# Kernel tuning notes

Measured on AMD Instinct MI355X. Metric: run time of the kernel, lower is better.

The kernel has to match this reference:

```python
import jax, jax.numpy as jnp
import numpy as np

NUM_HEADS = 8
EPS = 1e-9


def setup_inputs() -> dict:
    key = jax.random.key(0)
    ks = jax.random.split(key, 5)
    B, S, D = 2, 2048, 512
    x = jax.random.normal(ks[0], (B, S, D), dtype=jnp.float32)
    Wq = jax.random.normal(ks[1], (D, D), dtype=jnp.float32) * (1.0 / np.sqrt(D))
    Wk = jax.random.normal(ks[2], (D, D), dtype=jnp.float32) * (1.0 / np.sqrt(D))
    Wv = jax.random.normal(ks[3], (D, D), dtype=jnp.float32) * (1.0 / np.sqrt(D))
    Wo = jax.random.normal(ks[4], (D, D), dtype=jnp.float32) * (1.0 / np.sqrt(D))
    gamma = jnp.ones((D,), dtype=jnp.float32)
    beta = jnp.zeros((D,), dtype=jnp.float32)
    return {"x": x, "Wq": Wq, "Wk": Wk, "Wv": Wv, "Wo": Wo, "gamma": gamma, "beta": beta}


def _layernorm(x, gamma, beta):
    mean = jnp.mean(x, axis=-1, keepdims=True)
    var = jnp.mean(jnp.square(x - mean), axis=-1, keepdims=True)
    return gamma * ((x - mean) * jax.lax.rsqrt(var + EPS)) + beta


def reference(x, Wq, Wk, Wv, Wo, gamma, beta):
    B, S, D = x.shape
    H = NUM_HEADS
    dh = D // H
    # Note: in the original, K_V=(inputs, inputs) is captured BEFORE LayerNorm,
    # so only Q is layer-normalized; K and V use the raw inputs.
    q_in = _layernorm(x, gamma, beta)
    Q = jnp.einsum('bsd,de->bse', q_in, Wq).reshape(B, S, H, dh)
    K = jnp.einsum('bsd,de->bse', x, Wk).reshape(B, S, H, dh)
    V = jnp.einsum('bsd,de->bse', x, Wv).reshape(B, S, H, dh)
    # scaled dot-product attention (bias = 0, dropout disabled since dropout=1)
    scores = jnp.einsum('bqhd,bkhd->bhqk', Q, K) / jnp.sqrt(jnp.float32(dh))
    attn = jax.nn.softmax(scores, axis=-1)
    ctx = jnp.einsum('bhqk,bkhd->bqhd', attn, V).reshape(B, S, D)
    out = jnp.einsum('bsd,de->bse', ctx, Wo) + x  # output proj + residual
    return out
```

## Files before the change

kernel.cpp:

```cpp
#include <hip/hip_runtime.h>

typedef __bf16 bf16x8 __attribute__((ext_vector_type(8)));
typedef float f32x4 __attribute__((ext_vector_type(4)));

#define SCALE_LOG2E 0.18033688011112042f

__device__ __forceinline__ float bf2f(unsigned int u) { return __uint_as_float(u << 16); }
__device__ __forceinline__ unsigned short f2bfu(float f) {
    union { __bf16 h; unsigned short u; } v;
    v.h = (__bf16)f;
    return v.u;
}
__device__ __forceinline__ unsigned int pk2bf(float a, float b) {
    union { __bf16 h[2]; unsigned int u; } v;
    v.h[0] = (__bf16)a; v.h[1] = (__bf16)b;
    return v.u;
}

__device__ int probe_bf16(const void* xp) {
    const unsigned short* u = (const unsigned short*)xp;
    int cnt = 0;
    for (int i = 0; i < 128; i++) {
        unsigned e = (u[i] >> 7) & 0xFFu;
        cnt += (e == 0u || (e >= 0x6Cu && e <= 0x8Au)) ? 1 : 0;
    }
    return cnt >= 120;
}

__global__ __launch_bounds__(64)
void probe_k(const void* __restrict__ x, const void* __restrict__ Wq, int* __restrict__ flags) {
    if (threadIdx.x == 0) {
        flags[0] = probe_bf16(x);
        flags[1] = probe_bf16(Wq);
    }
}

__device__ __forceinline__ void load8f(const void* p, int isb, size_t idx, float* o) {
    if (isb) {
        uint4 v = *(const uint4*)((const unsigned short*)p + idx);
        o[0] = bf2f(v.x & 0xffffu); o[1] = bf2f(v.x >> 16);
        o[2] = bf2f(v.y & 0xffffu); o[3] = bf2f(v.y >> 16);
        o[4] = bf2f(v.z & 0xffffu); o[5] = bf2f(v.z >> 16);
        o[6] = bf2f(v.w & 0xffffu); o[7] = bf2f(v.w >> 16);
    } else {
        const float* f = (const float*)p + idx;
        float4 a = *(const float4*)f;
        float4 b = *(const float4*)(f + 4);
        o[0] = a.x; o[1] = a.y; o[2] = a.z; o[3] = a.w;
        o[4] = b.x; o[5] = b.y; o[6] = b.z; o[7] = b.w;
    }
}
__device__ __forceinline__ void load2f(const void* p, int isb, size_t idx, float& a, float& b) {
    if (isb) {
        unsigned int v = *(const unsigned int*)((const unsigned short*)p + idx);
        a = bf2f(v & 0xffffu); b = bf2f(v >> 16);
    } else {
        float2 f = *(const float2*)((const float*)p + idx);
        a = f.x; b = f.y;
    }
}
__device__ __forceinline__ float load1f(const void* p, int isb, size_t idx) {
    return isb ? bf2f((unsigned int)((const unsigned short*)p)[idx]) : ((const float*)p)[idx];
}

__global__ __launch_bounds__(256)
void setup_k(const void* __restrict__ x, const void* __restrict__ Wq, const void* __restrict__ Wk,
             const void* __restrict__ Wv, const void* __restrict__ Wo,
             const void* __restrict__ gamma, const void* __restrict__ beta,
             float* __restrict__ rowstats, float* __restrict__ gf, float* __restrict__ bfv,
             unsigned short* __restrict__ WT, const int* __restrict__ flags) {
    const int t = threadIdx.x;
    const int bid = blockIdx.x;
    if (bid < 1024) {
        const int isb = flags[1];
        __shared__ float tile[32][33];
        const int which = bid >> 8, tl = bid & 255;
        const int bx = (tl & 15) * 32, by = (tl >> 4) * 32;
        const void* W = (which == 0) ? Wq : (which == 1) ? Wk : (which == 2) ? Wv : Wo;
        unsigned short* dst = WT + (size_t)which * 512 * 512;
        const int xx = t & 31, y0 = t >> 5;
#pragma unroll
        for (int i = 0; i < 4; i++) {
            int y = y0 + i * 8;
            tile[y][xx] = load1f(W, isb, (size_t)(by + y) * 512 + bx + xx);
        }
        __syncthreads();
#pragma unroll
        for (int i = 0; i < 4; i++) {
            int y = y0 + i * 8;
            dst[(size_t)(bx + y) * 512 + by + xx] = f2bfu(tile[xx][y]);
        }
        return;
    }
    const int isb = flags[0];
    if (bid >= 5120) {
        const void* src = (bid == 5120) ? gamma : beta;
        float* dst = (bid == 5120) ? gf : bfv;
        float a, b;
        load2f(src, isb, (size_t)t * 2, a, b);
        dst[t * 2] = a; dst[t * 2 + 1] = b;
        return;
    }
    const int row = bid - 1024;
    float a, b;
    load2f(x, isb, (size_t)row * 512 + t * 2, a, b);
    float s = a + b, sq = a * a + b * b;
#pragma unroll
    for (int msk = 1; msk < 64; msk <<= 1) {
        s += __shfl_xor(s, msk);
        sq += __shfl_xor(sq, msk);
    }
    __shared__ float red[8];
    if ((t & 63) == 0) { red[t >> 6] = s; red[4 + (t >> 6)] = sq; }
    __syncthreads();
    if (t == 0) {
        float S = red[0] + red[1] + red[2] + red[3];
        float SQ = red[4] + red[5] + red[6] + red[7];
        float mean = S * (1.0f / 512.0f);
        float var = SQ * (1.0f / 512.0f) - mean * mean;
        rowstats[2 * row] = mean;
        rowstats[2 * row + 1] = rsqrtf(fmaxf(var, 0.0f) + 1e-9f);
    }
}

__global__ __launch_bounds__(256)
void proj_all_k(const void* __restrict__ x, const unsigned short* __restrict__ WT,
                const float* __restrict__ rowstats, const float* __restrict__ gf,
                const float* __restrict__ bfv, unsigned short* __restrict__ Qb,
                unsigned short* __restrict__ Kb, unsigned short* __restrict__ VtF,
                const int* __restrict__ flags) {
    __shared__ unsigned short As[128 * 40];
    __shared__ unsigned short Bs[128 * 40];
    __shared__ float Gs[512], Bts[512];
    const int t = threadIdx.x;
    const int isb = flags[0];
    const int w = t >> 6, lane = t & 63;
    const int quad = lane >> 4, ln = lane & 15;

    if (blockIdx.z == 0) {
        const int role = blockIdx.x & 1;
        const int n0 = (blockIdx.x >> 1) * 128;
        const int m0 = blockIdx.y * 128;
        const unsigned short* BT = WT + (size_t)role * 512 * 512;
        unsigned short* out = role ? Kb : Qb;
        const int wm = w & 1, wn = w >> 1;
        Gs[t] = gf[t]; Gs[t + 256] = gf[t + 256];
        Bts[t] = bfv[t]; Bts[t + 256] = bfv[t + 256];

        f32x4 acc[4][4];
        const f32x4 zero = {0.f, 0.f, 0.f, 0.f};
#pragma unroll
        for (int i = 0; i < 4; i++)
#pragma unroll
            for (int j = 0; j < 4; j++) acc[i][j] = zero;

        for (int kt = 0; kt < 512; kt += 32) {
            __syncthreads();
#pragma unroll
            for (int i = 0; i < 2; i++) {
                int o = t + i * 256;
                int r = o >> 2, c8 = o & 3;
                size_t gidx = (size_t)(m0 + r) * 512 + kt + c8 * 8;
                if (isb && role == 1) {
                    *(uint4*)(&As[r * 40 + c8 * 8]) = *(const uint4*)((const unsigned short*)x + gidx);
                } else {
                    float f[8];
                    load8f(x, isb, gidx, f);
                    if (role == 0) {
                        float mean = rowstats[2 * (m0 + r)];
                        float inv = rowstats[2 * (m0 + r) + 1];
#pragma unroll
                        for (int j = 0; j < 8; j++) {
                            int k = kt + c8 * 8 + j;
                            f[j] = (f[j] - mean) * inv * Gs[k] + Bts[k];
                        }
                    }
                    unsigned int pk[4];
#pragma unroll
                    for (int j = 0; j < 4; j++) pk[j] = pk2bf(f[2 * j], f[2 * j + 1]);
                    *(uint4*)(&As[r * 40 + c8 * 8]) = make_uint4(pk[0], pk[1], pk[2], pk[3]);
                }
                *(uint4*)(&Bs[r * 40 + c8 * 8]) = *(const uint4*)(BT + (size_t)(n0 + r) * 512 + kt + c8 * 8);
            }
            __syncthreads();
            bf16x8 af[4], bfr[4];
#pragma unroll
            for (int i = 0; i < 4; i++) {
                af[i] = *(const bf16x8*)(&As[(wm * 64 + i * 16 + ln) * 40 + quad * 8]);
                bfr[i] = *(const bf16x8*)(&Bs[(wn * 64 + i * 16 + ln) * 40 + quad * 8]);
            }
#pragma unroll
            for (int i = 0; i < 4; i++)
#pragma unroll
                for (int j = 0; j < 4; j++)
                    acc[i][j] = __builtin_amdgcn_mfma_f32_16x16x32_bf16(af[i], bfr[j], acc[i][j], 0, 0, 0);
        }
#pragma unroll
        for (int i = 0; i < 4; i++)
#pragma unroll
            for (int j = 0; j < 4; j++)
#pragma unroll
                for (int r = 0; r < 4; r++) {
                    int grow = m0 + wm * 64 + i * 16 + quad * 4 + r;
                    int gcol = n0 + wn * 64 + j * 16 + ln;
                    float v = acc[i][j][r];
                    if (role == 0) v *= SCALE_LOG2E;
                    out[(size_t)grow * 512 + gcol] = f2bfu(v);
                }
    } else {
        const int m0 = blockIdx.x * 64;
        const int n0 = blockIdx.y * 128;
        const unsigned short* AW = WT + (size_t)2 * 512 * 512;

        f32x4 acc[8];
        const f32x4 zero = {0.f, 0.f, 0.f, 0.f};
#pragma unroll
        for (int j = 0; j < 8; j++) acc[j] = zero;

        for (int kt = 0; kt < 512; kt += 32) {
            __syncthreads();
            {
                int r = t >> 2, c8 = t & 3;
                *(uint4*)(&As[r * 40 + c8 * 8]) = *(const uint4*)(AW + (size_t)(m0 + r) * 512 + kt + c8 * 8);
            }
#pragma unroll
            for (int i = 0; i < 2; i++) {
                int o = t + i * 256;
                int r = o >> 2, c8 = o & 3;
                size_t gidx = (size_t)(n0 + r) * 512 + kt + c8 * 8;
                if (isb) {
                    *(uint4*)(&Bs[r * 40 + c8 * 8]) = *(const uint4*)((const unsigned short*)x + gidx);
                } else {
                    float f[8];
                    load8f(x, isb, gidx, f);
                    unsigned int pk[4];
#pragma unroll
                    for (int j = 0; j < 4; j++) pk[j] = pk2bf(f[2 * j], f[2 * j + 1]);
                    *(uint4*)(&Bs[r * 40 + c8 * 8]) = make_uint4(pk[0], pk[1], pk[2], pk[3]);
                }
            }
            __syncthreads();
            bf16x8 af = *(const bf16x8*)(&As[(w * 16 + ln) * 40 + quad * 8]);
#pragma unroll
            for (int j = 0; j < 8; j++) {
                bf16x8 bfr = *(const bf16x8*)(&Bs[(j * 16 + ln) * 40 + quad * 8]);
                acc[j] = __builtin_amdgcn_mfma_f32_16x16x32_bf16(af, bfr, acc[j], 0, 0, 0);
            }
        }
#pragma unroll
        for (int j = 0; j < 8; j++)
#pragma unroll
            for (int r = 0; r < 4; r++) {
                int grow = m0 + w * 16 + quad * 4 + r;
                int gcol = n0 + j * 16 + ln;
                VtF[(size_t)grow * 4096 + gcol] = f2bfu(acc[j][r]);
            }
    }
}

__global__ __launch_bounds__(1024, 8)
void attn_m_k(const unsigned short* __restrict__ Qb, const unsigned short* __restrict__ Kb,
              const unsigned short* __restrict__ VtF, unsigned short* __restrict__ ctx) {
    const int S = 2048, PT = 72;
    const int t = threadIdx.x;
    const int qb = blockIdx.x, h = blockIdx.y, b = blockIdx.z;
    const int w = t >> 6, lane = t & 63;
    const int quad = lane >> 4, ln = lane & 15;
    const int qs = w & 3, kq = w >> 2;
    const int kh2 = kq & 1, ntp = kq >> 1;

    __shared__ unsigned short sh[384 * 72];
    unsigned short* const Qs  = sh;
    unsigned short* const KsA = sh + 64 * 72;
    unsigned short* const KsB = sh + 128 * 72;
    unsigned short* const VtA = sh + 192 * 72;
    unsigned short* const VtB = sh + 256 * 72;
    unsigned short* const PsA = sh;
    unsigned short* const PsB = sh + 320 * 72;

    const size_t baseQ  = (size_t)(b * S + qb * 64) * 512 + h * 64;
    const size_t baseK  = (size_t)(b * S) * 512 + h * 64;
    const size_t baseVt = (size_t)(h * 64) * 4096 + (size_t)b * S;

    const int r64 = (t & 511) >> 3, c8 = t & 7;

    const int stoff = r64 * PT + c8 * 8;
    const int kfo0  = (kq * 16 + ln) * PT + quad * 8;
    const int pso   = (qs * 16 + ln) * PT + kq * 16 + quad * 4;
    const int apo   = (qs * 16 + ln) * PT + kh2 * 32 + quad * 8;
    const int vbo0  = (ntp * 2 * 16 + ln) * PT + kh2 * 32 + quad * 8;

    const unsigned short* const gK = Kb + baseK + (size_t)r64 * 512 + c8 * 8;
    const unsigned short* const gV = VtF + baseVt + (size_t)r64 * 4096 + c8 * 8;

    if (t < 512)
        *(uint4*)(&Qs[stoff]) = *(const uint4*)(Qb + baseQ + (size_t)r64 * 512 + c8 * 8);
    __syncthreads();
    bf16x8 qf[2];
#pragma unroll
    for (int i = 0; i < 2; i++)
        qf[i] = *(const bf16x8*)(&Qs[(qs * 16 + ln) * PT + quad * 8 + 32 * i]);

    f32x4 acc[2];
    const f32x4 zero = {0.f, 0.f, 0.f, 0.f};
    acc[0] = zero; acc[1] = zero;
    float lsum = 0.f;

    uint4 sreg;
    if (t < 512) sreg = *(const uint4*)(gK);
    else         sreg = *(const uint4*)(gV);

#define ATTN_TILE(KS, VT, PS, ...)                                                      \
    {                                                                                   \
        if (t < 512) *(uint4*)(&KS[stoff]) = sreg;                                      \
        else         *(uint4*)(&VT[stoff]) = sreg;                                      \
        __syncthreads();                                           \
        __VA_ARGS__                                      \
        f32x4 sc = zero;                                                                \
        sc = __builtin_amdgcn_mfma_f32_16x16x32_bf16(                                   \
            *(const bf16x8*)(&KS[kfo0]), qf[0], sc, 0, 0, 0);                           \
        sc = __builtin_amdgcn_mfma_f32_16x16x32_bf16(                                   \
            *(const bf16x8*)(&KS[kfo0 + 32]), qf[1], sc, 0, 0, 0);                      \
        float e0 = __builtin_amdgcn_exp2f(fminf(sc[0], 30.f));                          \
        float e1 = __builtin_amdgcn_exp2f(fminf(sc[1], 30.f));                          \
        float e2 = __builtin_amdgcn_exp2f(fminf(sc[2], 30.f));                          \
        float e3 = __builtin_amdgcn_exp2f(fminf(sc[3], 30.f));                          \
        lsum += (e0 + e1) + (e2 + e3);                                                  \
        *(uint2*)(&PS[pso]) = make_uint2(pk2bf(e0, e1), pk2bf(e2, e3));                 \
        __syncthreads();                 \
        bf16x8 ap = *(const bf16x8*)(&PS[apo]);                                         \
        acc[0] = __builtin_amdgcn_mfma_f32_16x16x32_bf16(                               \
            ap, *(const bf16x8*)(&VT[vbo0]), acc[0], 0, 0, 0);                          \
        acc[1] = __builtin_amdgcn_mfma_f32_16x16x32_bf16(                               \
            ap, *(const bf16x8*)(&VT[vbo0 + 16 * PT]), acc[1], 0, 0, 0);                \
    }

    for (int kc = 0; kc < S; kc += 128) {
        ATTN_TILE(KsA, VtA, PsA, {
            if (t < 512) sreg = *(const uint4*)(gK + (size_t)(kc + 64) * 512);
            else         sreg = *(const uint4*)(gV + kc + 64);
        })
        ATTN_TILE(KsB, VtB, PsB, {
            if (kc + 128 < S) {
                if (t < 512) sreg = *(const uint4*)(gK + (size_t)(kc + 128) * 512);
                else         sreg = *(const uint4*)(gV + kc + 128);
            }
        })
    }
#undef ATTN_TILE

    lsum += __shfl_xor(lsum, 16);
    lsum += __shfl_xor(lsum, 32);

    __syncthreads();
    float* scr  = (float*)sh;
    float* lred = scr + 4096;
    if (quad == 0) lred[kq * 64 + qs * 16 + ln] = lsum;
    if (kh2 == 1) {
#pragma unroll
        for (int ntl = 0; ntl < 2; ntl++)
#pragma unroll
            for (int r = 0; r < 4; r++)
                scr[(qs * 16 + quad * 4 + r) * 64 + (ntp * 2 + ntl) * 16 + ln] = acc[ntl][r];
    }
    __syncthreads();
    if (kh2 == 0) {
        const size_t baseO = (size_t)(b * S + qb * 64 + qs * 16 + quad * 4) * 512 + h * 64 + ln;
#pragma unroll
        for (int r = 0; r < 4; r++) {
            int qrow = qs * 16 + quad * 4 + r;
            float lt = lred[qrow] + lred[64 + qrow] + lred[128 + qrow] + lred[192 + qrow];
            float inv = 1.0f / lt;
#pragma unroll
            for (int ntl = 0; ntl < 2; ntl++) {
                int nt = ntp * 2 + ntl;
                float v = acc[ntl][r] + scr[qrow * 64 + nt * 16 + ln];
                ctx[baseO + (size_t)r * 512 + nt * 16] = f2bfu(v * inv);
            }
        }
    }
}

__global__ __launch_bounds__(256)
void outproj_k(const unsigned short* __restrict__ ctx, const unsigned short* __restrict__ BT,
               const void* __restrict__ x, void* __restrict__ outp, const int* __restrict__ flags) {
    __shared__ unsigned short As[128 * 40];
    __shared__ unsigned short Bs[64 * 40];
    const int t = threadIdx.x;
    const int isb = flags[0];
    const int m0 = blockIdx.y * 128, n0 = blockIdx.x * 64;
    const int w = t >> 6, lane = t & 63;
    const int wm = w & 1, wn = w >> 1;
    const int quad = lane >> 4, ln = lane & 15;

    f32x4 acc[4][2];
    const f32x4 zero = {0.f, 0.f, 0.f, 0.f};
#pragma unroll
    for (int i = 0; i < 4; i++)
#pragma unroll
        for (int j = 0; j < 2; j++) acc[i][j] = zero;

    for (int kt = 0; kt < 512; kt += 32) {
        __syncthreads();
#pragma unroll
        for (int i = 0; i < 2; i++) {
            int o = t + i * 256;
            int r = o >> 2, c8 = o & 3;
            *(uint4*)(&As[r * 40 + c8 * 8]) = *(const uint4*)(ctx + (size_t)(m0 + r) * 512 + kt + c8 * 8);
        }
        {
            int r = t >> 2, c8 = t & 3;
            *(uint4*)(&Bs[r * 40 + c8 * 8]) = *(const uint4*)(BT + (size_t)(n0 + r) * 512 + kt + c8 * 8);
        }
        __syncthreads();
        bf16x8 af[4], bfr[2];
#pragma unroll
        for (int i = 0; i < 4; i++)
            af[i] = *(const bf16x8*)(&As[(wm * 64 + i * 16 + ln) * 40 + quad * 8]);
#pragma unroll
        for (int j = 0; j < 2; j++)
            bfr[j] = *(const bf16x8*)(&Bs[(wn * 32 + j * 16 + ln) * 40 + quad * 8]);
#pragma unroll
        for (int i = 0; i < 4; i++)
#pragma unroll
            for (int j = 0; j < 2; j++)
                acc[i][j] = __builtin_amdgcn_mfma_f32_16x16x32_bf16(af[i], bfr[j], acc[i][j], 0, 0, 0);
    }
#pragma unroll
    for (int i = 0; i < 4; i++)
#pragma unroll
        for (int j = 0; j < 2; j++)
#pragma unroll
            for (int r = 0; r < 4; r++) {
                int grow = m0 + wm * 64 + i * 16 + quad * 4 + r;
                int gcol = n0 + wn * 32 + j * 16 + ln;
                size_t idx = (size_t)grow * 512 + gcol;
                float v = acc[i][j][r] + load1f(x, isb, idx);
                if (isb) ((unsigned short*)outp)[idx] = f2bfu(v);
                else     ((float*)outp)[idx] = v;
            }
}

__global__ __launch_bounds__(256)
void fill_k(unsigned short* out, int n) {
    int i = blockIdx.x * 256 + threadIdx.x;
    if (i < n) out[i] = 0x4442;
}

extern "C" void kernel_launch(void* const* d_in, const int* in_sizes, int n_in,
                              void* d_out, int out_size, void* d_ws, size_t ws_size,
                              hipStream_t stream) {
    const void* x     = d_in[0];
    const void* Wq    = d_in[1];
    const void* Wk    = d_in[2];
    const void* Wv    = d_in[3];
    const void* Wo    = d_in[4];
    const void* gamma = d_in[5];
    const void* beta  = d_in[6];

    const size_t NW = 512 * 512;
    const size_t NX = 4096 * 512;
    char* w = (char*)d_ws;

    const size_t FULL_STATS_OFF = 2097152 + 3 * NX * 2;
    const size_t NEED_FULL = FULL_STATS_OFF + 32768 + 4096 + 16;

    if (ws_size < NEED_FULL) {
        fill_k<<<(out_size + 255) / 256, 256, 0, stream>>>((unsigned short*)d_out, out_size);
        return;
    }

    unsigned short* WT  = (unsigned short*)w;
    unsigned short* Qb  = (unsigned short*)(w + 2097152);
    unsigned short* Kb  = Qb + NX;
    unsigned short* VtF = Kb + NX;
    unsigned short* ctx = Qb;
    float* rowstats = (float*)(w + FULL_STATS_OFF);
    float* gf = rowstats + 8192;
    float* bfv = gf + 512;
    int* flags = (int*)(bfv + 512);

    probe_k<<<1, 64, 0, stream>>>(x, Wq, flags);
    setup_k<<<5122, 256, 0, stream>>>(x, Wq, Wk, Wv, Wo, gamma, beta, rowstats, gf, bfv, WT, flags);
    proj_all_k<<<dim3(8, 32, 2), 256, 0, stream>>>(x, WT, rowstats, gf, bfv, Qb, Kb, VtF, flags);
    attn_m_k<<<dim3(32, 8, 2), 1024, 0, stream>>>(Qb, Kb, VtF, ctx);
    outproj_k<<<dim3(8, 32), 256, 0, stream>>>(ctx, WT + 3 * NW, x, d_out, flags);
}
```

Before: 166.7 us.

## Keep softmax probabilities in registers and split PV across key-quarter warps

The attention kernel no longer writes the exp'd scores to shared memory for a cross-warp reshuffle. Each warp keeps its own P fragment in registers and uses it directly as the A operand of the PV MFMA, pairing two consecutive K tiles so the k-dimension lines up. It then computes all four 64-column output tiles, producing a partial sum over its key quarter, and these partials are reduced through shared memory at the end. This removes one barrier and the P shared-memory round trip per tile, at the cost of four V buffers, more accumulator registers and a larger final reduction.

```diff
diff --git a/kernel.cpp b/kernel.cpp
--- a/kernel.cpp
+++ b/kernel.cpp
@@ -261,22 +261,21 @@
 __global__ __launch_bounds__(1024, 8)
 void attn_m_k(const unsigned short* __restrict__ Qb, const unsigned short* __restrict__ Kb,
               const unsigned short* __restrict__ VtF, unsigned short* __restrict__ ctx) {
-    const int S = 2048, PT = 72;
+    const int S = 2048, PT = 72, NT = 32;
     const int t = threadIdx.x;
     const int qb = blockIdx.x, h = blockIdx.y, b = blockIdx.z;
     const int w = t >> 6, lane = t & 63;
     const int quad = lane >> 4, ln = lane & 15;
     const int qs = w & 3, kq = w >> 2;
-    const int kh2 = kq & 1, ntp = kq >> 1;
-
-    __shared__ unsigned short sh[384 * 72];
+
+    __shared__ unsigned short sh[32256];
     unsigned short* const Qs  = sh;
-    unsigned short* const KsA = sh + 64 * 72;
-    unsigned short* const KsB = sh + 128 * 72;
-    unsigned short* const VtA = sh + 192 * 72;
-    unsigned short* const VtB = sh + 256 * 72;
-    unsigned short* const PsA = sh;
-    unsigned short* const PsB = sh + 320 * 72;
+    unsigned short* const KsA = sh + 4608;
+    unsigned short* const KsB = sh + 9216;
+    unsigned short* const Vt0 = sh + 13824;
+    unsigned short* const Vt1 = sh + 18432;
+    unsigned short* const Vt2 = sh + 23040;
+    unsigned short* const Vt3 = sh + 27648;
 
     const size_t baseQ  = (size_t)(b * S + qb * 64) * 512 + h * 64;
     const size_t baseK  = (size_t)(b * S) * 512 + h * 64;
@@ -286,12 +285,14 @@
 
     const int stoff = r64 * PT + c8 * 8;
     const int kfo0  = (kq * 16 + ln) * PT + quad * 8;
-    const int pso   = (qs * 16 + ln) * PT + kq * 16 + quad * 4;
-    const int apo   = (qs * 16 + ln) * PT + kh2 * 32 + quad * 8;
-    const int vbo0  = (ntp * 2 * 16 + ln) * PT + kh2 * 32 + quad * 8;
+    const int vto   = ln * PT + kq * 16 + quad * 4;
 
     const unsigned short* const gK = Kb + baseK + (size_t)r64 * 512 + c8 * 8;
     const unsigned short* const gV = VtF + baseVt + (size_t)r64 * 4096 + c8 * 8;
+
+    uint4 sreg;
+    if (t < 512) sreg = *(const uint4*)(gK);
+    else         sreg = *(const uint4*)(gV);
 
     if (t < 512)
         *(uint4*)(&Qs[stoff]) = *(const uint4*)(Qb + baseQ + (size_t)r64 * 512 + c8 * 8);
@@ -301,80 +302,104 @@
     for (int i = 0; i < 2; i++)
         qf[i] = *(const bf16x8*)(&Qs[(qs * 16 + ln) * PT + quad * 8 + 32 * i]);
 
-    f32x4 acc[2];
+    f32x4 acc[4];
     const f32x4 zero = {0.f, 0.f, 0.f, 0.f};
-    acc[0] = zero; acc[1] = zero;
+#pragma unroll
+    for (int j = 0; j < 4; j++) acc[j] = zero;
     float lsum = 0.f;
 
-    uint4 sreg;
-    if (t < 512) sreg = *(const uint4*)(gK);
-    else         sreg = *(const uint4*)(gV);
-
-#define ATTN_TILE(KS, VT, PS, ...)                                                      \
-    {                                                                                   \
-        if (t < 512) *(uint4*)(&KS[stoff]) = sreg;                                      \
-        else         *(uint4*)(&VT[stoff]) = sreg;                                      \
-        __syncthreads();                                           \
-        __VA_ARGS__                                      \
-        f32x4 sc = zero;                                                                \
-        sc = __builtin_amdgcn_mfma_f32_16x16x32_bf16(                                   \
-            *(const bf16x8*)(&KS[kfo0]), qf[0], sc, 0, 0, 0);                           \
-        sc = __builtin_amdgcn_mfma_f32_16x16x32_bf16(                                   \
-            *(const bf16x8*)(&KS[kfo0 + 32]), qf[1], sc, 0, 0, 0);                      \
-        float e0 = __builtin_amdgcn_exp2f(fminf(sc[0], 30.f));                          \
-        float e1 = __builtin_amdgcn_exp2f(fminf(sc[1], 30.f));                          \
-        float e2 = __builtin_amdgcn_exp2f(fminf(sc[2], 30.f));                          \
-        float e3 = __builtin_amdgcn_exp2f(fminf(sc[3], 30.f));                          \
-        lsum += (e0 + e1) + (e2 + e3);                                                  \
-        *(uint2*)(&PS[pso]) = make_uint2(pk2bf(e0, e1), pk2bf(e2, e3));                 \
-        __syncthreads();                 \
-        bf16x8 ap = *(const bf16x8*)(&PS[apo]);                                         \
-        acc[0] = __builtin_amdgcn_mfma_f32_16x16x32_bf16(                               \
-            ap, *(const bf16x8*)(&VT[vbo0]), acc[0], 0, 0, 0);                          \
-        acc[1] = __builtin_amdgcn_mfma_f32_16x16x32_bf16(                               \
-            ap, *(const bf16x8*)(&VT[vbo0 + 16 * PT]), acc[1], 0, 0, 0);                \
-    }
-
-    for (int kc = 0; kc < S; kc += 128) {
-        ATTN_TILE(KsA, VtA, PsA, {
-            if (t < 512) sreg = *(const uint4*)(gK + (size_t)(kc + 64) * 512);
-            else         sreg = *(const uint4*)(gV + kc + 64);
-        })
-        ATTN_TILE(KsB, VtB, PsB, {
-            if (kc + 128 < S) {
-                if (t < 512) sreg = *(const uint4*)(gK + (size_t)(kc + 128) * 512);
-                else         sreg = *(const uint4*)(gV + kc + 128);
-            }
-        })
-    }
-#undef ATTN_TILE
+#define STAGE(KS, VT)                                                       \
+    {                                                                       \
+        if (t < 512) *(uint4*)(&KS[stoff]) = sreg;                          \
+        else         *(uint4*)(&VT[stoff]) = sreg;                          \
+    }
+#define PRELOAD(kt)                                                         \
+    if ((kt) < NT) {                                                        \
+        if (t < 512) sreg = *(const uint4*)(gK + (size_t)(kt) * 32768);     \
+        else         sreg = *(const uint4*)(gV + (size_t)(kt) * 64);        \
+    }
+#define QK_EXP(KS, U0, U1)                                                  \
+    {                                                                       \
+        f32x4 sc = zero;                                                    \
+        sc = __builtin_amdgcn_mfma_f32_16x16x32_bf16(                       \
+            *(const bf16x8*)(&KS[kfo0]), qf[0], sc, 0, 0, 0);               \
+        sc = __builtin_amdgcn_mfma_f32_16x16x32_bf16(                       \
+            *(const bf16x8*)(&KS[kfo0 + 32]), qf[1], sc, 0, 0, 0);          \
+        float e0 = __builtin_amdgcn_exp2f(fminf(sc[0], 30.f));              \
+        float e1 = __builtin_amdgcn_exp2f(fminf(sc[1], 30.f));              \
+        float e2 = __builtin_amdgcn_exp2f(fminf(sc[2], 30.f));              \
+        float e3 = __builtin_amdgcn_exp2f(fminf(sc[3], 30.f));              \
+        lsum += (e0 + e1) + (e2 + e3);                                      \
+        U0 = pk2bf(e0, e1); U1 = pk2bf(e2, e3);                             \
+    }
+#define PV4(VTE, VTO)                                                       \
+    {                                                                       \
+        union { unsigned int u[4]; bf16x8 v; } ap;                          \
+        ap.u[0] = uA0; ap.u[1] = uA1; ap.u[2] = uB0; ap.u[3] = uB1;         \
+        _Pragma("unroll")                                                   \
+        for (int nt = 0; nt < 4; nt++) {                                    \
+            union { unsigned int u[4]; bf16x8 v; } vb;                      \
+            *(uint2*)(&vb.u[0]) = *(const uint2*)(&VTE[vto + nt * 16 * PT]); \
+            *(uint2*)(&vb.u[2]) = *(const uint2*)(&VTO[vto + nt * 16 * PT]); \
+            acc[nt] = __builtin_amdgcn_mfma_f32_16x16x32_bf16(ap.v, vb.v, acc[nt], 0, 0, 0); \
+        }                                                                   \
+    }
+
+    for (int m = 0; m < 8; m++) {
+        const int T = m * 4;
+        unsigned int uA0, uA1, uB0, uB1;
+        STAGE(KsA, Vt0);
+        __syncthreads();
+        PRELOAD(T + 1);
+        QK_EXP(KsA, uA0, uA1);
+        STAGE(KsB, Vt1);
+        __syncthreads();
+        PRELOAD(T + 2);
+        QK_EXP(KsB, uB0, uB1);
+        PV4(Vt0, Vt1);
+        __syncthreads();
+        STAGE(KsA, Vt2);
+        __syncthreads();
+        PRELOAD(T + 3);
+        QK_EXP(KsA, uA0, uA1);
+        STAGE(KsB, Vt3);
+        __syncthreads();
+        PRELOAD(T + 4);
+        QK_EXP(KsB, uB0, uB1);
+        PV4(Vt2, Vt3);
+        __syncthreads();
+    }
+#undef STAGE
+#undef PRELOAD
+#undef QK_EXP
+#undef PV4
 
     lsum += __shfl_xor(lsum, 16);
     lsum += __shfl_xor(lsum, 32);
 
+    float* scr  = (float*)sh;
+    float* lred = scr + 13056;
+    if (quad == 0) lred[kq * 64 + qs * 16 + ln] = lsum;
+    if (kq != 0) {
+        const int pb = (kq - 1) * 4352 + (qs * 16 + quad * 4) * 68 + ln;
+#pragma unroll
+        for (int nt = 0; nt < 4; nt++)
+#pragma unroll
+            for (int r = 0; r < 4; r++)
+                scr[pb + r * 68 + nt * 16] = acc[nt][r];
+    }
     __syncthreads();
-    float* scr  = (float*)sh;
-    float* lred = scr + 4096;
-    if (quad == 0) lred[kq * 64 + qs * 16 + ln] = lsum;
-    if (kh2 == 1) {
-#pragma unroll
-        for (int ntl = 0; ntl < 2; ntl++)
-#pragma unroll
-            for (int r = 0; r < 4; r++)
-                scr[(qs * 16 + quad * 4 + r) * 64 + (ntp * 2 + ntl) * 16 + ln] = acc[ntl][r];
-    }
-    __syncthreads();
-    if (kh2 == 0) {
+    if (kq == 0) {
         const size_t baseO = (size_t)(b * S + qb * 64 + qs * 16 + quad * 4) * 512 + h * 64 + ln;
 #pragma unroll
         for (int r = 0; r < 4; r++) {
             int qrow = qs * 16 + quad * 4 + r;
             float lt = lred[qrow] + lred[64 + qrow] + lred[128 + qrow] + lred[192 + qrow];
             float inv = 1.0f / lt;
-#pragma unroll
-            for (int ntl = 0; ntl < 2; ntl++) {
-                int nt = ntp * 2 + ntl;
-                float v = acc[ntl][r] + scr[qrow * 64 + nt * 16 + ln];
+            int rb = qrow * 68 + ln;
+#pragma unroll
+            for (int nt = 0; nt < 4; nt++) {
+                float v = acc[nt][r] + scr[rb + nt * 16] + scr[4352 + rb + nt * 16] + scr[8704 + rb + nt * 16];
                 ctx[baseO + (size_t)r * 512 + nt * 16] = f2bfu(v * inv);
             }
         }
```

Result: no change. 169.8 us (+1.8%).
